# Kernel optimization log

Measured on AMD Instinct MI355X. Metric: run time of the kernel, lower is better.

The kernel has to match this reference:

```python
import jax, jax.numpy as jnp
import numpy as np

N = 50000
E = 600000


def gcn_conv(x, W, b, src, dst, n):
    # PyG GCNConv: h = x @ W; add self-loops; symmetric normalization; aggregate; + bias
    h = x @ W  # [N, out]
    deg = jnp.zeros((n,), h.dtype).at[dst].add(1.0) + 1.0  # self-loop included
    dinv = jax.lax.rsqrt(deg)  # deg >= 1, always finite
    coef = dinv[src] * dinv[dst]  # [E]
    msg = h[src] * coef[:, None]  # [E, out]  (the memory-bound gather)
    agg = jax.ops.segment_sum(msg, dst, num_segments=n)
    agg = agg + h * (dinv * dinv)[:, None]  # self-loop contribution
    return agg + b


def setup_inputs() -> dict:
    key = jax.random.key(0)
    ks = jax.random.split(key, 8)
    x = jax.random.normal(ks[0], (N, 128), dtype=jnp.float32)
    edge_index = jax.random.randint(ks[1], (2, E), 0, N, dtype=jnp.int64 if jax.config.jax_enable_x64 else jnp.int32)
    def glorot(k, fan_in, fan_out):
        s = jnp.sqrt(6.0 / (fan_in + fan_out))
        return jax.random.uniform(k, (fan_in, fan_out), jnp.float32, -s, s)
    W1 = glorot(ks[2], 128, 128)
    b1 = jnp.zeros((128,), jnp.float32)
    W2 = glorot(ks[3], 128, 64)
    b2 = jnp.zeros((64,), jnp.float32)
    W3 = glorot(ks[4], 64, 16)
    b3 = jnp.zeros((16,), jnp.float32)
    return {"x": x, "edge_index": edge_index, "W1": W1, "b1": b1, "W2": W2, "b2": b2, "W3": W3, "b3": b3}


def reference(x, edge_index, W1, b1, W2, b2, W3, b3):
    src, dst = edge_index[0], edge_index[1]
    n = x.shape[0]
    h = jax.nn.relu(gcn_conv(x, W1, b1, src, dst, n))
    h = jax.nn.relu(gcn_conv(h, W2, b2, src, dst, n))
    h = gcn_conv(h, W3, b3, src, dst, n)
    return h
```

## Files before the change

### kernel.cpp

```cpp
#include <hip/hip_runtime.h>
#include <hip/hip_fp16.h>
#include <type_traits>


typedef _Float16 f16x8 __attribute__((ext_vector_type(8)));
typedef float f32x4 __attribute__((ext_vector_type(4)));

#define CSR_CAP 32

__device__ inline float2 h2f(unsigned int u) {
  __half2 h = __builtin_bit_cast(__half2, u);
  return __half22float2(h);
}

__device__ inline void fma8h(float4& a0, float4& a1, const uint4& g, float w) {
  float2 f0 = h2f(g.x), f1 = h2f(g.y), f2 = h2f(g.z), f3 = h2f(g.w);
  a0.x = fmaf(f0.x, w, a0.x);
  a0.y = fmaf(f0.y, w, a0.y);
  a0.z = fmaf(f1.x, w, a0.z);
  a0.w = fmaf(f1.y, w, a0.w);
  a1.x = fmaf(f2.x, w, a1.x);
  a1.y = fmaf(f2.y, w, a1.y);
  a1.z = fmaf(f3.x, w, a1.z);
  a1.w = fmaf(f3.y, w, a1.w);
}

__device__ inline unsigned int pack2h(float x, float y) {
  __half2 h = __floats2half2_rn(x, y);
  return __builtin_bit_cast(unsigned int, h);
}

__device__ inline uint2 pack4h(const float4& v) {
  uint2 r;
  r.x = pack2h(v.x, v.y);
  r.y = pack2h(v.z, v.w);
  return r;
}

template <int K, int F, typename TIN>
__global__ __launch_bounds__(512) void gemm_mfma(const TIN* __restrict__ A,
                                                 const float* __restrict__ W,
                                                 __half* __restrict__ C16, int n,
                                                 int nwaves,
                                                 const int* __restrict__ src,
                                                 const int* __restrict__ dst,
                                                 int* __restrict__ cur,
                                                 unsigned short* __restrict__ csr,
                                                 int E) {
  constexpr int KP = K + 8;
  constexpr int KS = K / 32;
  constexpr int NT = F / 16;

  __shared__ __half Ws[F * KP];

  int t = threadIdx.x;

  if (t >= 256) {
    __syncthreads();
    int base = blockIdx.x * 256 + (t - 256);
    int stride = gridDim.x * 256;
    for (int e0 = base; e0 < E; e0 += 4 * stride) {
      int d[4], s[4];
      bool v[4];
#pragma unroll
      for (int u = 0; u < 4; ++u) {
        int e = e0 + u * stride;
        v[u] = e < E;
        int ee = v[u] ? e : 0;
        d[u] = dst[ee];
        s[u] = src[ee];
      }
      int pos[4];
#pragma unroll
      for (int u = 0; u < 4; ++u)
        if (v[u]) pos[u] = atomicAdd(&cur[d[u]], 1);
#pragma unroll
      for (int u = 0; u < 4; ++u)
        if (v[u]) {
          int p = pos[u] >= CSR_CAP ? CSR_CAP - 1 : pos[u];
          csr[(size_t)d[u] * CSR_CAP + p] = (unsigned short)s[u];
        }
    }
    return;
  }

  for (int i = t; i < K * F; i += 256) {
    int kk = i / F, nn = i % F;
    Ws[nn * KP + kk] = __float2half(W[i]);
  }
  __syncthreads();

  int wave = blockIdx.x * 4 + (t >> 6);
  if (wave >= nwaves) return;
  int lane = t & 63;
  int m = lane & 15;
  int quad = lane >> 4;

  int arow = wave * 16 + m;
  if (arow >= n) arow = n - 1;

  f16x8 af[KS];
  if constexpr (std::is_same_v<TIN, float>) {
#pragma unroll
    for (int ks = 0; ks < KS; ++ks) {
      const float* p = A + (size_t)arow * K + ks * 32 + quad * 8;
      float4 lo = *(const float4*)p;
      float4 hi = *(const float4*)(p + 4);
      f16x8 a;
      a[0] = (_Float16)lo.x; a[1] = (_Float16)lo.y;
      a[2] = (_Float16)lo.z; a[3] = (_Float16)lo.w;
      a[4] = (_Float16)hi.x; a[5] = (_Float16)hi.y;
      a[6] = (_Float16)hi.z; a[7] = (_Float16)hi.w;
      af[ks] = a;
    }
  } else {
#pragma unroll
    for (int ks = 0; ks < KS; ++ks)
      af[ks] = *(const f16x8*)(const void*)&A[(size_t)arow * K + ks * 32 + quad * 8];
  }

  f32x4 acc[NT];
#pragma unroll
  for (int nt = 0; nt < NT; ++nt) acc[nt] = (f32x4){0.f, 0.f, 0.f, 0.f};
#pragma unroll
  for (int nt = 0; nt < NT; ++nt)
#pragma unroll
    for (int ks = 0; ks < KS; ++ks) {
      f16x8 b = *(const f16x8*)(const void*)&Ws[(nt * 16 + m) * KP + ks * 32 + quad * 8];
      acc[nt] = __builtin_amdgcn_mfma_f32_16x16x32_f16(af[ks], b, acc[nt], 0, 0, 0);
    }

  int rbase = wave * 16 + quad * 4;
#pragma unroll
  for (int nt = 0; nt < NT; ++nt)
#pragma unroll
    for (int r = 0; r < 4; ++r) {
      int rr = rbase + r;
      if (rr < n) C16[(size_t)rr * F + nt * 16 + m] = __float2half(acc[nt][r]);
    }
}

template <int K, int F, int CPL, int EU>
__global__ __launch_bounds__(512) void aggmm(
    const __half* __restrict__ hprev, const float* __restrict__ W,
    const float* __restrict__ bias, const int* __restrict__ cnt,
    const unsigned short* __restrict__ csr, __half* __restrict__ C16, int n) {
  constexpr int KP = K + 8;
  constexpr int KS = K / 32;
  constexpr int NT = F / 16;
  constexpr int TPN = 8;
  constexpr int RS = K / 8;
  static_assert(TPN * CPL == RS, "chunk coverage");

  __shared__ __half Ws[F * KP];
  __shared__ __half As[64 * KP];

  int t = threadIdx.x;
  for (int i = t; i < K * F; i += 512) {
    int kk = i / F, nn = i % F;
    Ws[nn * KP + kk] = __float2half(W[i]);
  }

  int wid = t >> 6;
  int lane = t & 63;
  int nb = blockIdx.x * 64;

  {
    int sub = lane / TPN;
    int fl = lane % TPN;
    int nib = wid * 8 + sub;
    int node = nb + nib;
    int nd = node < n ? node : n - 1;
    const uint4* h4 = (const uint4*)hprev;
    int c0 = cnt[nd];
    float di = rsqrtf((float)c0 + 1.0f);
    float sc = di * di;
    int cc = c0 < CSR_CAP ? c0 : CSR_CAP;
    float4 acc[CPL][2];
#pragma unroll
    for (int c = 0; c < CPL; ++c) {
      acc[c][0] = make_float4(0.f, 0.f, 0.f, 0.f);
      acc[c][1] = make_float4(0.f, 0.f, 0.f, 0.f);
    }
#pragma unroll
    for (int c = 0; c < CPL; ++c) {
      uint4 sv = h4[(size_t)nd * RS + fl + c * TPN];
      fma8h(acc[c][0], acc[c][1], sv, sc);
    }
    int j = nd * CSR_CAP;
    int e = j + cc;
    int p[EU];
#pragma unroll
    for (int u = 0; u < EU; ++u) p[u] = csr[j + u];
    for (; j + EU <= e;) {
      uint4 g[EU][CPL];
#pragma unroll
      for (int u = 0; u < EU; ++u)
#pragma unroll
        for (int c = 0; c < CPL; ++c) g[u][c] = h4[(size_t)p[u] * RS + fl + c * TPN];
      int cs[EU];
#pragma unroll
      for (int u = 0; u < EU; ++u) cs[u] = cnt[p[u]];
      j += EU;
      int pn[EU];
#pragma unroll
      for (int u = 0; u < EU; ++u) pn[u] = csr[j + u];
#pragma unroll
      for (int u = 0; u < EU; ++u) {
        float w = rsqrtf((float)cs[u] + 1.0f) * di;
#pragma unroll
        for (int c = 0; c < CPL; ++c) fma8h(acc[c][0], acc[c][1], g[u][c], w);
      }
#pragma unroll
      for (int u = 0; u < EU; ++u) p[u] = pn[u];
    }
#pragma unroll
    for (int u = 0; u < EU; ++u) {
      if (j + u < e) {
        float w = rsqrtf((float)cnt[p[u]] + 1.0f) * di;
#pragma unroll
        for (int c = 0; c < CPL; ++c) {
          uint4 g = h4[(size_t)p[u] * RS + fl + c * TPN];
          fma8h(acc[c][0], acc[c][1], g, w);
        }
      }
    }
#pragma unroll
    for (int c = 0; c < CPL; ++c) {
      int ch = fl + c * TPN;
      float4 b0 = *(const float4*)&bias[ch * 8];
      float4 b1 = *(const float4*)&bias[ch * 8 + 4];
      float4 r0 = make_float4(fmaxf(acc[c][0].x + b0.x, 0.f), fmaxf(acc[c][0].y + b0.y, 0.f),
                              fmaxf(acc[c][0].z + b0.z, 0.f), fmaxf(acc[c][0].w + b0.w, 0.f));
      float4 r1 = make_float4(fmaxf(acc[c][1].x + b1.x, 0.f), fmaxf(acc[c][1].y + b1.y, 0.f),
                              fmaxf(acc[c][1].z + b1.z, 0.f), fmaxf(acc[c][1].w + b1.w, 0.f));
      uint2 lo = pack4h(r0), hi = pack4h(r1);
      uint4 pk;
      pk.x = lo.x; pk.y = lo.y; pk.z = hi.x; pk.w = hi.y;
      *(uint4*)&As[(size_t)nib * KP + ch * 8] = pk;
    }
  }

  __syncthreads();

  if (wid < 4) {
    int m = lane & 15;
    int quad = lane >> 4;
    const __half* At = &As[(size_t)wid * 16 * KP];
    f16x8 af[KS];
#pragma unroll
    for (int ks = 0; ks < KS; ++ks)
      af[ks] = *(const f16x8*)(const void*)&At[m * KP + ks * 32 + quad * 8];

    f32x4 acc2[NT];
#pragma unroll
    for (int nt = 0; nt < NT; ++nt) acc2[nt] = (f32x4){0.f, 0.f, 0.f, 0.f};
#pragma unroll
    for (int nt = 0; nt < NT; ++nt)
#pragma unroll
      for (int ks = 0; ks < KS; ++ks) {
        f16x8 bfr = *(const f16x8*)(const void*)&Ws[(nt * 16 + m) * KP + ks * 32 + quad * 8];
        acc2[nt] = __builtin_amdgcn_mfma_f32_16x16x32_f16(af[ks], bfr, acc2[nt], 0, 0, 0);
      }

    int rbase = nb + wid * 16 + quad * 4;
#pragma unroll
    for (int nt = 0; nt < NT; ++nt)
#pragma unroll
      for (int r = 0; r < 4; ++r) {
        int rr = rbase + r;
        if (rr < n) C16[(size_t)rr * F + nt * 16 + m] = __float2half(acc2[nt][r]);
      }
  }
}

__global__ __launch_bounds__(256) void agg_final(
    const __half* __restrict__ h16, const int* __restrict__ cnt,
    const unsigned short* __restrict__ csr, const float* __restrict__ bias,
    float* __restrict__ out, int n) {
  int node = blockIdx.x * 64 + threadIdx.x / 4;
  int q = threadIdx.x & 3;
  int half = q >> 1;
  int fl = q & 1;
  bool valid = node < n;
  int nd = valid ? node : n - 1;

  const uint4* h4 = (const uint4*)h16;
  int c0 = cnt[nd];
  float di = rsqrtf((float)c0 + 1.0f);
  int cc = c0 < CSR_CAP ? c0 : CSR_CAP;
  float4 a0 = make_float4(0.f, 0.f, 0.f, 0.f);
  float4 a1 = make_float4(0.f, 0.f, 0.f, 0.f);
  if (half == 0) {
    uint4 sv = h4[(size_t)nd * 2 + fl];
    fma8h(a0, a1, sv, di * di);
  }
  int s = nd * CSR_CAP;
  int e = s + cc;
  int j = s + half;
  for (; j + 2 < e; j += 4) {
    int p0 = csr[j];
    int p1 = csr[j + 2];
    int ca = cnt[p0];
    int cb = cnt[p1];
    uint4 g0 = h4[(size_t)p0 * 2 + fl];
    uint4 g1 = h4[(size_t)p1 * 2 + fl];
    fma8h(a0, a1, g0, rsqrtf((float)ca + 1.0f) * di);
    fma8h(a0, a1, g1, rsqrtf((float)cb + 1.0f) * di);
  }
  for (; j < e; j += 2) {
    int p = csr[j];
    uint4 g = h4[(size_t)p * 2 + fl];
    fma8h(a0, a1, g, rsqrtf((float)cnt[p] + 1.0f) * di);
  }

  a0.x += __shfl_xor(a0.x, 2);
  a0.y += __shfl_xor(a0.y, 2);
  a0.z += __shfl_xor(a0.z, 2);
  a0.w += __shfl_xor(a0.w, 2);
  a1.x += __shfl_xor(a1.x, 2);
  a1.y += __shfl_xor(a1.y, 2);
  a1.z += __shfl_xor(a1.z, 2);
  a1.w += __shfl_xor(a1.w, 2);

  if (valid && half == 0) {
    float4 b0 = *(const float4*)&bias[fl * 8];
    float4 b1 = *(const float4*)&bias[fl * 8 + 4];
    float4 r0 = make_float4(a0.x + b0.x, a0.y + b0.y, a0.z + b0.z, a0.w + b0.w);
    float4 r1 = make_float4(a1.x + b1.x, a1.y + b1.y, a1.z + b1.z, a1.w + b1.w);
    float* op = &out[(size_t)node * 16 + fl * 8];
    *(float4*)op = r0;
    *(float4*)(op + 4) = r1;
  }
}


extern "C" void kernel_launch(void* const* d_in, const int* in_sizes, int n_in,
                              void* d_out, int out_size, void* d_ws, size_t ws_size,
                              hipStream_t stream) {
  const float* x = (const float*)d_in[0];
  const int* edge = (const int*)d_in[1];
  const float* W1 = (const float*)d_in[2];
  const float* b1 = (const float*)d_in[3];
  const float* W2 = (const float*)d_in[4];
  const float* b2 = (const float*)d_in[5];
  const float* W3 = (const float*)d_in[6];
  const float* b3 = (const float*)d_in[7];

  const int N = in_sizes[0] / 128;
  const int E = in_sizes[1] / 2;
  const int* src = edge;
  const int* dstp = edge + E;
  float* out = (float*)d_out;

  size_t off = 0;
  auto take = [&](size_t bytes) -> void* {
    void* r = (char*)d_ws + off;
    off += (bytes + 255) & ~(size_t)255;
    return r;
  };
  int* cur = (int*)take((size_t)N * 4);
  unsigned short* csr =
      (unsigned short*)take((size_t)N * CSR_CAP * 2 + 256);
  __half* t1 = (__half*)take((size_t)N * 128 * 2);
  __half* t2 = (__half*)take((size_t)N * 64 * 2);
  __half* t3 = (__half*)take((size_t)N * 16 * 2);

  hipMemsetAsync(d_ws, 0, ((size_t)N * 4 + 255) & ~(size_t)255, stream);

  int nwaves = (N + 15) / 16;
  int gblk = (nwaves + 3) / 4;
  int fblk = (N + 63) / 64;

  gemm_mfma<128, 128, float><<<gblk, 512, 0, stream>>>(x, W1, t1, N, nwaves,
                                                       src, dstp, cur, csr, E);

  aggmm<128, 64, 2, 4><<<fblk, 512, 0, stream>>>(t1, W2, b1, cur, csr, t2, N);
  aggmm<64, 16, 1, 4><<<fblk, 512, 0, stream>>>(t2, W3, b2, cur, csr, t3, N);
  agg_final<<<fblk, 256, 0, stream>>>(t3, cur, csr, b3, out, N);
}
```

Before: 175.6 us.

## Fuse last three layers into one persistent kernel with grid barriers

Replaces the two aggmm launches and the agg_final launch with a single 512-block persistent kernel. Each block processes two 64-node tiles per stage, and a software grid barrier (an atomic counter zeroed by the existing memset) separates the stages. This removes two kernel launches and their inter-kernel gaps, and loads W2 and W3 into shared memory once per block instead of once per tile. The cost is that the grid-wide barrier requires all 512 blocks to be co-resident, and its guard-limited spin can break out before every block arrives. It also fixes the launch at 512 blocks, so correctness depends on N ≤ 65536.

```diff
diff --git a/kernel.cpp b/kernel.cpp
--- a/kernel.cpp
+++ b/kernel.cpp
@@ -35,6 +35,19 @@
   r.x = pack2h(v.x, v.y);
   r.y = pack2h(v.z, v.w);
   return r;
+}
+
+__device__ inline void grid_barrier(int* bar, int target) {
+  __syncthreads();
+  if (threadIdx.x == 0) {
+    __hip_atomic_fetch_add(bar, 1, __ATOMIC_RELEASE, __HIP_MEMORY_SCOPE_AGENT);
+    int guard = 0;
+    while (__hip_atomic_load(bar, __ATOMIC_ACQUIRE, __HIP_MEMORY_SCOPE_AGENT) < target) {
+      __builtin_amdgcn_s_sleep(16);
+      if (++guard > (1 << 21)) break;
+    }
+  }
+  __syncthreads();
 }
 
 template <int K, int F, typename TIN>
@@ -141,10 +154,10 @@
 }
 
 template <int K, int F, int CPL, int EU>
-__global__ __launch_bounds__(512) void aggmm(
-    const __half* __restrict__ hprev, const float* __restrict__ W,
-    const float* __restrict__ bias, const int* __restrict__ cnt,
-    const unsigned short* __restrict__ csr, __half* __restrict__ C16, int n) {
+__device__ __forceinline__ void aggmm_tile(
+    const __half* __restrict__ hprev, const float* __restrict__ bias,
+    const int* __restrict__ cnt, const unsigned short* __restrict__ csr,
+    __half* __restrict__ C16, int n, int nb, __half* Ws, __half* As) {
   constexpr int KP = K + 8;
   constexpr int KS = K / 32;
   constexpr int NT = F / 16;
@@ -152,18 +165,9 @@
   constexpr int RS = K / 8;
   static_assert(TPN * CPL == RS, "chunk coverage");
 
-  __shared__ __half Ws[F * KP];
-  __shared__ __half As[64 * KP];
-
   int t = threadIdx.x;
-  for (int i = t; i < K * F; i += 512) {
-    int kk = i / F, nn = i % F;
-    Ws[nn * KP + kk] = __float2half(W[i]);
-  }
-
   int wid = t >> 6;
   int lane = t & 63;
-  int nb = blockIdx.x * 64;
 
   {
     int sub = lane / TPN;
@@ -272,65 +276,104 @@
         if (rr < n) C16[(size_t)rr * F + nt * 16 + m] = __float2half(acc2[nt][r]);
       }
   }
-}
-
-__global__ __launch_bounds__(256) void agg_final(
-    const __half* __restrict__ h16, const int* __restrict__ cnt,
-    const unsigned short* __restrict__ csr, const float* __restrict__ bias,
-    float* __restrict__ out, int n) {
-  int node = blockIdx.x * 64 + threadIdx.x / 4;
-  int q = threadIdx.x & 3;
-  int half = q >> 1;
-  int fl = q & 1;
-  bool valid = node < n;
-  int nd = valid ? node : n - 1;
-
-  const uint4* h4 = (const uint4*)h16;
-  int c0 = cnt[nd];
-  float di = rsqrtf((float)c0 + 1.0f);
-  int cc = c0 < CSR_CAP ? c0 : CSR_CAP;
-  float4 a0 = make_float4(0.f, 0.f, 0.f, 0.f);
-  float4 a1 = make_float4(0.f, 0.f, 0.f, 0.f);
-  if (half == 0) {
-    uint4 sv = h4[(size_t)nd * 2 + fl];
-    fma8h(a0, a1, sv, di * di);
-  }
-  int s = nd * CSR_CAP;
-  int e = s + cc;
-  int j = s + half;
-  for (; j + 2 < e; j += 4) {
-    int p0 = csr[j];
-    int p1 = csr[j + 2];
-    int ca = cnt[p0];
-    int cb = cnt[p1];
-    uint4 g0 = h4[(size_t)p0 * 2 + fl];
-    uint4 g1 = h4[(size_t)p1 * 2 + fl];
-    fma8h(a0, a1, g0, rsqrtf((float)ca + 1.0f) * di);
-    fma8h(a0, a1, g1, rsqrtf((float)cb + 1.0f) * di);
-  }
-  for (; j < e; j += 2) {
-    int p = csr[j];
-    uint4 g = h4[(size_t)p * 2 + fl];
-    fma8h(a0, a1, g, rsqrtf((float)cnt[p] + 1.0f) * di);
-  }
-
-  a0.x += __shfl_xor(a0.x, 2);
-  a0.y += __shfl_xor(a0.y, 2);
-  a0.z += __shfl_xor(a0.z, 2);
-  a0.w += __shfl_xor(a0.w, 2);
-  a1.x += __shfl_xor(a1.x, 2);
-  a1.y += __shfl_xor(a1.y, 2);
-  a1.z += __shfl_xor(a1.z, 2);
-  a1.w += __shfl_xor(a1.w, 2);
-
-  if (valid && half == 0) {
-    float4 b0 = *(const float4*)&bias[fl * 8];
-    float4 b1 = *(const float4*)&bias[fl * 8 + 4];
-    float4 r0 = make_float4(a0.x + b0.x, a0.y + b0.y, a0.z + b0.z, a0.w + b0.w);
-    float4 r1 = make_float4(a1.x + b1.x, a1.y + b1.y, a1.z + b1.z, a1.w + b1.w);
-    float* op = &out[(size_t)node * 16 + fl * 8];
-    *(float4*)op = r0;
-    *(float4*)(op + 4) = r1;
+
+  __syncthreads();
+}
+
+__global__ __launch_bounds__(512, 4) void fused_tail(
+    const __half* __restrict__ t1, __half* __restrict__ t2,
+    __half* __restrict__ t3, const float* __restrict__ W2,
+    const float* __restrict__ b1, const float* __restrict__ W3,
+    const float* __restrict__ b2, const float* __restrict__ b3,
+    float* __restrict__ out, const int* __restrict__ cnt,
+    const unsigned short* __restrict__ csr, int n, int* __restrict__ bar) {
+  __shared__ __half Ws[64 * 136];
+  __shared__ __half As[64 * 136];
+
+  int t = threadIdx.x;
+  int grid = gridDim.x;
+
+  for (int i = t; i < 128 * 64; i += 512) {
+    int kk = i / 64, nn = i % 64;
+    Ws[nn * 136 + kk] = __float2half(W2[i]);
+  }
+#pragma unroll 1
+  for (int k = 0; k < 2; ++k) {
+    int nb = (blockIdx.x + k * grid) * 64;
+    if (nb < n) aggmm_tile<128, 64, 2, 4>(t1, b1, cnt, csr, t2, n, nb, Ws, As);
+  }
+
+  grid_barrier(bar, grid);
+
+  for (int i = t; i < 64 * 16; i += 512) {
+    int kk = i / 16, nn = i % 16;
+    Ws[nn * 72 + kk] = __float2half(W3[i]);
+  }
+#pragma unroll 1
+  for (int k = 0; k < 2; ++k) {
+    int nb = (blockIdx.x + k * grid) * 64;
+    if (nb < n) aggmm_tile<64, 16, 1, 4>(t2, b2, cnt, csr, t3, n, nb, Ws, As);
+  }
+
+  grid_barrier(bar, 2 * grid);
+
+  {
+    int nb = blockIdx.x * 128;
+    if (nb >= n) return;
+    int node = nb + (t >> 2);
+    int q = t & 3;
+    int half = q >> 1;
+    int fl = q & 1;
+    bool valid = node < n;
+    int nd = valid ? node : n - 1;
+
+    const uint4* h4 = (const uint4*)t3;
+    int c0 = cnt[nd];
+    float di = rsqrtf((float)c0 + 1.0f);
+    int cc = c0 < CSR_CAP ? c0 : CSR_CAP;
+    float4 a0 = make_float4(0.f, 0.f, 0.f, 0.f);
+    float4 a1 = make_float4(0.f, 0.f, 0.f, 0.f);
+    if (half == 0) {
+      uint4 sv = h4[(size_t)nd * 2 + fl];
+      fma8h(a0, a1, sv, di * di);
+    }
+    int s = nd * CSR_CAP;
+    int e = s + cc;
+    int j = s + half;
+    for (; j + 2 < e; j += 4) {
+      int p0 = csr[j];
+      int p1 = csr[j + 2];
+      int ca = cnt[p0];
+      int cb = cnt[p1];
+      uint4 g0 = h4[(size_t)p0 * 2 + fl];
+      uint4 g1 = h4[(size_t)p1 * 2 + fl];
+      fma8h(a0, a1, g0, rsqrtf((float)ca + 1.0f) * di);
+      fma8h(a0, a1, g1, rsqrtf((float)cb + 1.0f) * di);
+    }
+    for (; j < e; j += 2) {
+      int p = csr[j];
+      uint4 g = h4[(size_t)p * 2 + fl];
+      fma8h(a0, a1, g, rsqrtf((float)cnt[p] + 1.0f) * di);
+    }
+
+    a0.x += __shfl_xor(a0.x, 2);
+    a0.y += __shfl_xor(a0.y, 2);
+    a0.z += __shfl_xor(a0.z, 2);
+    a0.w += __shfl_xor(a0.w, 2);
+    a1.x += __shfl_xor(a1.x, 2);
+    a1.y += __shfl_xor(a1.y, 2);
+    a1.z += __shfl_xor(a1.z, 2);
+    a1.w += __shfl_xor(a1.w, 2);
+
+    if (valid && half == 0) {
+      float4 b0 = *(const float4*)&b3[fl * 8];
+      float4 b1v = *(const float4*)&b3[fl * 8 + 4];
+      float4 r0 = make_float4(a0.x + b0.x, a0.y + b0.y, a0.z + b0.z, a0.w + b0.w);
+      float4 r1 = make_float4(a1.x + b1v.x, a1.y + b1v.y, a1.z + b1v.z, a1.w + b1v.w);
+      float* op = &out[(size_t)node * 16 + fl * 8];
+      *(float4*)op = r0;
+      *(float4*)(op + 4) = r1;
+    }
   }
 }
 
@@ -360,22 +403,22 @@
     return r;
   };
   int* cur = (int*)take((size_t)N * 4);
+  int* bar = (int*)take(4);
+  size_t zlen = off;
   unsigned short* csr =
       (unsigned short*)take((size_t)N * CSR_CAP * 2 + 256);
   __half* t1 = (__half*)take((size_t)N * 128 * 2);
   __half* t2 = (__half*)take((size_t)N * 64 * 2);
   __half* t3 = (__half*)take((size_t)N * 16 * 2);
 
-  hipMemsetAsync(d_ws, 0, ((size_t)N * 4 + 255) & ~(size_t)255, stream);
+  hipMemsetAsync(d_ws, 0, zlen, stream);
 
   int nwaves = (N + 15) / 16;
   int gblk = (nwaves + 3) / 4;
-  int fblk = (N + 63) / 64;
 
   gemm_mfma<128, 128, float><<<gblk, 512, 0, stream>>>(x, W1, t1, N, nwaves,
                                                        src, dstp, cur, csr, E);
 
-  aggmm<128, 64, 2, 4><<<fblk, 512, 0, stream>>>(t1, W2, b1, cur, csr, t2, N);
-  aggmm<64, 16, 1, 4><<<fblk, 512, 0, stream>>>(t2, W3, b2, cur, csr, t3, N);
-  agg_final<<<fblk, 256, 0, stream>>>(t3, cur, csr, b3, out, N);
-}
+  fused_tail<<<512, 512, 0, stream>>>(t1, t2, t3, W2, b1, W3, b2, b3, out,
+                                      cur, csr, N, bar);
+}
```

New measurement: 339.7 us. 93.5% more time.

## Split each node's edge list across two lane halves in aggmm

Applied to the files above, without the earlier changes.

The aggregation stage now gives each node 16 lanes in two halves of 8. Each half walks alternate edges of the node's CSR list, and the halves' partial sums are combined with a cross-lane xor-shuffle before bias, ReLU and the store to shared memory. Blocks now cover 32 nodes instead of 64, doubling the grid, and only two waves run the MFMA stage. The aim is more memory-level parallelism per node and a shorter per-node dependency chain, at the cost of more blocks, repeated loading of W into shared memory per block, and fewer waves doing the matrix multiply.

```diff
diff --git a/kernel.cpp b/kernel.cpp
--- a/kernel.cpp
+++ b/kernel.cpp
@@ -148,12 +148,11 @@
   constexpr int KP = K + 8;
   constexpr int KS = K / 32;
   constexpr int NT = F / 16;
-  constexpr int TPN = 8;
   constexpr int RS = K / 8;
-  static_assert(TPN * CPL == RS, "chunk coverage");
+  static_assert(8 * CPL == RS, "chunk coverage (8 chunk-lanes per half)");
 
   __shared__ __half Ws[F * KP];
-  __shared__ __half As[64 * KP];
+  __shared__ __half As[32 * KP];
 
   int t = threadIdx.x;
   for (int i = t; i < K * F; i += 512) {
@@ -163,12 +162,14 @@
 
   int wid = t >> 6;
   int lane = t & 63;
-  int nb = blockIdx.x * 64;
+  int nb = blockIdx.x * 32;
 
   {
-    int sub = lane / TPN;
-    int fl = lane % TPN;
-    int nib = wid * 8 + sub;
+    int ng = lane >> 4;
+    int sl = lane & 15;
+    int half = sl >> 3;
+    int fl = sl & 7;
+    int nib = wid * 4 + ng;
     int node = nb + nib;
     int nd = node < n ? node : n - 1;
     const uint4* h4 = (const uint4*)hprev;
@@ -182,29 +183,32 @@
       acc[c][0] = make_float4(0.f, 0.f, 0.f, 0.f);
       acc[c][1] = make_float4(0.f, 0.f, 0.f, 0.f);
     }
-#pragma unroll
-    for (int c = 0; c < CPL; ++c) {
-      uint4 sv = h4[(size_t)nd * RS + fl + c * TPN];
-      fma8h(acc[c][0], acc[c][1], sv, sc);
-    }
-    int j = nd * CSR_CAP;
-    int e = j + cc;
+    if (half == 0) {
+#pragma unroll
+      for (int c = 0; c < CPL; ++c) {
+        uint4 sv = h4[(size_t)nd * RS + fl + c * 8];
+        fma8h(acc[c][0], acc[c][1], sv, sc);
+      }
+    }
+    int j0 = nd * CSR_CAP;
+    int e = j0 + cc;
+    int j = j0 + half;
     int p[EU];
 #pragma unroll
-    for (int u = 0; u < EU; ++u) p[u] = csr[j + u];
-    for (; j + EU <= e;) {
+    for (int u = 0; u < EU; ++u) p[u] = csr[j + 2 * u];
+    for (; j + 2 * EU - 2 < e;) {
       uint4 g[EU][CPL];
 #pragma unroll
       for (int u = 0; u < EU; ++u)
 #pragma unroll
-        for (int c = 0; c < CPL; ++c) g[u][c] = h4[(size_t)p[u] * RS + fl + c * TPN];
+        for (int c = 0; c < CPL; ++c) g[u][c] = h4[(size_t)p[u] * RS + fl + c * 8];
       int cs[EU];
 #pragma unroll
       for (int u = 0; u < EU; ++u) cs[u] = cnt[p[u]];
-      j += EU;
+      j += 2 * EU;
       int pn[EU];
 #pragma unroll
-      for (int u = 0; u < EU; ++u) pn[u] = csr[j + u];
+      for (int u = 0; u < EU; ++u) pn[u] = csr[j + 2 * u];
 #pragma unroll
       for (int u = 0; u < EU; ++u) {
         float w = rsqrtf((float)cs[u] + 1.0f) * di;
@@ -216,34 +220,47 @@
     }
 #pragma unroll
     for (int u = 0; u < EU; ++u) {
-      if (j + u < e) {
+      if (j + 2 * u < e) {
         float w = rsqrtf((float)cnt[p[u]] + 1.0f) * di;
 #pragma unroll
         for (int c = 0; c < CPL; ++c) {
-          uint4 g = h4[(size_t)p[u] * RS + fl + c * TPN];
+          uint4 g = h4[(size_t)p[u] * RS + fl + c * 8];
           fma8h(acc[c][0], acc[c][1], g, w);
         }
       }
     }
 #pragma unroll
     for (int c = 0; c < CPL; ++c) {
-      int ch = fl + c * TPN;
-      float4 b0 = *(const float4*)&bias[ch * 8];
-      float4 b1 = *(const float4*)&bias[ch * 8 + 4];
-      float4 r0 = make_float4(fmaxf(acc[c][0].x + b0.x, 0.f), fmaxf(acc[c][0].y + b0.y, 0.f),
-                              fmaxf(acc[c][0].z + b0.z, 0.f), fmaxf(acc[c][0].w + b0.w, 0.f));
-      float4 r1 = make_float4(fmaxf(acc[c][1].x + b1.x, 0.f), fmaxf(acc[c][1].y + b1.y, 0.f),
-                              fmaxf(acc[c][1].z + b1.z, 0.f), fmaxf(acc[c][1].w + b1.w, 0.f));
-      uint2 lo = pack4h(r0), hi = pack4h(r1);
-      uint4 pk;
-      pk.x = lo.x; pk.y = lo.y; pk.z = hi.x; pk.w = hi.y;
-      *(uint4*)&As[(size_t)nib * KP + ch * 8] = pk;
+      acc[c][0].x += __shfl_xor(acc[c][0].x, 8);
+      acc[c][0].y += __shfl_xor(acc[c][0].y, 8);
+      acc[c][0].z += __shfl_xor(acc[c][0].z, 8);
+      acc[c][0].w += __shfl_xor(acc[c][0].w, 8);
+      acc[c][1].x += __shfl_xor(acc[c][1].x, 8);
+      acc[c][1].y += __shfl_xor(acc[c][1].y, 8);
+      acc[c][1].z += __shfl_xor(acc[c][1].z, 8);
+      acc[c][1].w += __shfl_xor(acc[c][1].w, 8);
+    }
+    if (half == 0) {
+#pragma unroll
+      for (int c = 0; c < CPL; ++c) {
+        int ch = fl + c * 8;
+        float4 b0 = *(const float4*)&bias[ch * 8];
+        float4 b1 = *(const float4*)&bias[ch * 8 + 4];
+        float4 r0 = make_float4(fmaxf(acc[c][0].x + b0.x, 0.f), fmaxf(acc[c][0].y + b0.y, 0.f),
+                                fmaxf(acc[c][0].z + b0.z, 0.f), fmaxf(acc[c][0].w + b0.w, 0.f));
+        float4 r1 = make_float4(fmaxf(acc[c][1].x + b1.x, 0.f), fmaxf(acc[c][1].y + b1.y, 0.f),
+                                fmaxf(acc[c][1].z + b1.z, 0.f), fmaxf(acc[c][1].w + b1.w, 0.f));
+        uint2 lo = pack4h(r0), hi = pack4h(r1);
+        uint4 pk;
+        pk.x = lo.x; pk.y = lo.y; pk.z = hi.x; pk.w = hi.y;
+        *(uint4*)&As[(size_t)nib * KP + ch * 8] = pk;
+      }
     }
   }
 
   __syncthreads();
 
-  if (wid < 4) {
+  if (wid < 2) {
     int m = lane & 15;
     int quad = lane >> 4;
     const __half* At = &As[(size_t)wid * 16 * KP];
@@ -370,12 +387,13 @@
 
   int nwaves = (N + 15) / 16;
   int gblk = (nwaves + 3) / 4;
+  int ablk = (N + 31) / 32;
   int fblk = (N + 63) / 64;
 
   gemm_mfma<128, 128, float><<<gblk, 512, 0, stream>>>(x, W1, t1, N, nwaves,
                                                        src, dstp, cur, csr, E);
 
-  aggmm<128, 64, 2, 4><<<fblk, 512, 0, stream>>>(t1, W2, b1, cur, csr, t2, N);
-  aggmm<64, 16, 1, 4><<<fblk, 512, 0, stream>>>(t2, W3, b2, cur, csr, t3, N);
+  aggmm<128, 64, 2, 4><<<ablk, 512, 0, stream>>>(t1, W2, b1, cur, csr, t2, N);
+  aggmm<64, 16, 1, 4><<<ablk, 512, 0, stream>>>(t2, W3, b2, cur, csr, t3, N);
   agg_final<<<fblk, 256, 0, stream>>>(t3, cur, csr, b3, out, N);
 }
```

Measured after the change: 172.6 us. About the same (-1.7%).
